# Kernel tuning notes

Hardware: AMD Instinct MI355X
Metric: run time of the kernel (lower is better)

Reference implementation:

```python
import jax, jax.numpy as jnp
import numpy as np


def setup_inputs() -> dict:
    key = jax.random.key(0)
    ks = jax.random.split(key, 12)
    N, F, H, E = 100000, 128, 128, 625000
    x = jax.random.normal(ks[0], (N, F), dtype=jnp.float32)
    edge_index = jax.random.randint(ks[1], (2, E), 0, N, dtype=jnp.int64)
    s1 = 1.0 / np.sqrt(2 * F)
    s2 = 1.0 / np.sqrt(H)
    W1 = jax.random.uniform(ks[2], (2 * F, H), jnp.float32, -s1, s1)
    b1 = jax.random.uniform(ks[3], (H,), jnp.float32, -s1, s1)
    W2 = jax.random.uniform(ks[4], (H, H), jnp.float32, -s2, s2)
    b2 = jax.random.uniform(ks[5], (H,), jnp.float32, -s2, s2)
    W3 = jax.random.uniform(ks[6], (H, H), jnp.float32, -s2, s2)
    b3 = jax.random.uniform(ks[7], (H,), jnp.float32, -s2, s2)
    W4 = jax.random.uniform(ks[8], (H, 1), jnp.float32, -s2, s2)
    b4 = jax.random.uniform(ks[9], (1,), jnp.float32, -s2, s2)
    return {"x": x, "edge_index": edge_index, "W1": W1, "b1": b1,
            "W2": W2, "b2": b2, "W3": W3, "b3": b3, "W4": W4, "b4": b4}


def reference(x, edge_index, W1, b1, W2, b2, W3, b3, W4, b4):
    # Gather endpoint features and concat -> [E, 2F]
    x_i = x[edge_index[0], :]
    x_j = x[edge_index[1], :]
    ef = jnp.concatenate([x_i, x_j], axis=-1)
    h = jax.nn.relu(ef @ W1 + b1)
    h = jax.nn.relu(h @ W2 + b2)
    h = jax.nn.relu(h @ W3 + b3)
    return jax.nn.sigmoid(h @ W4 + b4)  # [E, 1]
```

## Files before the change

### kernel.cpp

```cpp
#include <hip/hip_runtime.h>
#include <math.h>

typedef _Float16 half8 __attribute__((ext_vector_type(8)));
typedef _Float16 half4 __attribute__((ext_vector_type(4)));
typedef float f32x4 __attribute__((ext_vector_type(4)));

#define HDIM 128
#define WHALFS 65536
#define SCR_HALFS 2048
#define LDS_HALFS (WHALFS + 8 * SCR_HALFS)
#define LDS_BYTES (LDS_HALFS * 2)

__global__ __launch_bounds__(256) void prep_kernel(
    const float* __restrict__ x,  const float* __restrict__ W1,
    const float* __restrict__ W2, const float* __restrict__ W3,
    _Float16* __restrict__ xh,  _Float16* __restrict__ W1p,
    _Float16* __restrict__ W2p, _Float16* __restrict__ W3p, int NF)
{
    int bid = blockIdx.x;
    if (bid < 32) {
        int t = bid * 256 + threadIdx.x;
        const float* W; _Float16* Wp; int KS; int u;
        if (t < 4096)      { W = W1; Wp = W1p; KS = 8; u = t; }
        else if (t < 6144) { W = W2; Wp = W2p; KS = 4; u = t - 4096; }
        else               { W = W3; Wp = W3p; KS = 4; u = t - 6144; }
        int lane = u & 63;
        int fk   = u >> 6;
        int ks   = fk % KS;
        int ct   = fk / KS;
        int m    = ct * 16 + (lane & 15);
        int k0   = ks * 32 + (lane >> 4) * 8;
        half8 v;
        #pragma unroll
        for (int j = 0; j < 8; ++j) v[j] = (_Float16)W[(k0 + j) * HDIM + m];
        *(half8*)(Wp + (size_t)u * 8) = v;
    } else {
        const long stride = (long)(gridDim.x - 32) * 256;
        for (long u = (long)(bid - 32) * 256 + threadIdx.x; u * 8 < (long)NF; u += stride) {
            long i = u * 8;
            const float4* xf = (const float4*)(x + i);
            float4 f0 = xf[0], f1 = xf[1];
            half8 v;
            v[0] = (_Float16)f0.x; v[1] = (_Float16)f0.y;
            v[2] = (_Float16)f0.z; v[3] = (_Float16)f0.w;
            v[4] = (_Float16)f1.x; v[5] = (_Float16)f1.y;
            v[6] = (_Float16)f1.z; v[7] = (_Float16)f1.w;
            *(half8*)(xh + i) = v;
        }
    }
}

__device__ __forceinline__ void acc_bias_init(
    f32x4 (&acc)[2][8], const float* __restrict__ bias, int quad)
{
    #pragma unroll
    for (int ct = 0; ct < 8; ++ct) {
        float4 bv = *(const float4*)(bias + ct * 16 + quad * 4);
        f32x4 b = {bv.x, bv.y, bv.z, bv.w};
        acc[0][ct] = b;
        acc[1][ct] = b;
    }
}

__device__ __forceinline__ void epi_extract(
    f32x4 (&acc)[2][8], _Float16* __restrict__ scr, int l15, int quad, int sw,
    half8 (&bh)[2][4], const float* __restrict__ next_bias)
{
    #pragma unroll
    for (int nt = 0; nt < 2; ++nt) {
        #pragma unroll
        for (int ct = 0; ct < 8; ++ct) {
            half4 h;
            h[0] = (_Float16)fmaxf(acc[nt][ct][0], 0.f);
            h[1] = (_Float16)fmaxf(acc[nt][ct][1], 0.f);
            h[2] = (_Float16)fmaxf(acc[nt][ct][2], 0.f);
            h[3] = (_Float16)fmaxf(acc[nt][ct][3], 0.f);
            *(half4*)(scr + ((l15 * 128 + ct * 16 + quad * 4) ^ sw)) = h;
        }
        #pragma unroll
        for (int ks = 0; ks < 4; ++ks)
            bh[nt][ks] = *(const half8*)(scr + ((l15 * 128 + ks * 32 + quad * 8) ^ sw));
    }
    acc_bias_init(acc, next_bias, quad);
}

__device__ __forceinline__ void layer_mfma(
    f32x4 (&acc)[2][8], const _Float16* __restrict__ Wl,
    half8 (&bh)[2][4], int lane)
{
    __builtin_amdgcn_s_setprio(1);
    #pragma unroll
    for (int ks = 0; ks < 4; ++ks) {
        #pragma unroll
        for (int ch = 0; ch < 2; ++ch) {
            half8 aw[4];
            #pragma unroll
            for (int c = 0; c < 4; ++c)
                aw[c] = *(const half8*)(Wl + ((size_t)(((ch * 4 + c) * 4 + ks) * 64 + lane)) * 8);
            #pragma unroll
            for (int nt = 0; nt < 2; ++nt)
                #pragma unroll
                for (int c = 0; c < 4; ++c)
                    acc[nt][ch * 4 + c] = __builtin_amdgcn_mfma_f32_16x16x32_f16(
                        aw[c], bh[nt][ks], acc[nt][ch * 4 + c], 0, 0, 0);
        }
    }
    __builtin_amdgcn_s_setprio(0);
}

__device__ __forceinline__ void layer1_half(
    f32x4 (&acc)[2][8], const _Float16* __restrict__ W1l,
    half8 (&bef)[2][4], int ks0, int lane)
{
    __builtin_amdgcn_s_setprio(1);
    #pragma unroll
    for (int ks = 0; ks < 4; ++ks) {
        #pragma unroll
        for (int ch = 0; ch < 2; ++ch) {
            half8 aw[4];
            #pragma unroll
            for (int c = 0; c < 4; ++c)
                aw[c] = *(const half8*)(W1l + ((size_t)(((ch * 4 + c) * 8 + ks0 + ks) * 64 + lane)) * 8);
            #pragma unroll
            for (int nt = 0; nt < 2; ++nt)
                #pragma unroll
                for (int c = 0; c < 4; ++c)
                    acc[nt][ch * 4 + c] = __builtin_amdgcn_mfma_f32_16x16x32_f16(
                        aw[c], bef[nt][ks], acc[nt][ch * 4 + c], 0, 0, 0);
        }
    }
    __builtin_amdgcn_s_setprio(0);
}

__global__ __launch_bounds__(512, 2) void edge_mlp_kernel(
    const int* __restrict__ ei, const _Float16* __restrict__ xh,
    const _Float16* __restrict__ wpack,
    const float* __restrict__ b1, const float* __restrict__ b2,
    const float* __restrict__ b3, const float* __restrict__ W4,
    const float* __restrict__ b4, float* __restrict__ out, int E)
{
    extern __shared__ _Float16 lds[];

    {
        float4* dst = (float4*)lds;
        const float4* src = (const float4*)wpack;
        #pragma unroll
        for (int i = 0; i < 16; ++i)
            dst[i * 512 + threadIdx.x] = src[i * 512 + threadIdx.x];
    }
    __syncthreads();

    const int tid  = threadIdx.x;
    const int wave = tid >> 6;
    const int lane = tid & 63;
    const int l15  = lane & 15;
    const int quad = lane >> 4;
    const int sw   = (l15 & 7) << 3;

    const _Float16* W1l = lds;
    const _Float16* W2l = lds + 32768;
    const _Float16* W3l = lds + 49152;
    _Float16* scr = lds + WHALFS + wave * SCR_HALFS;

    const int ntiles = (E + 255) >> 8;
    const float b4v = b4[0];

    int gi[2], gj[2];
    {
        const int base0 = blockIdx.x * 256 + wave * 32;
        #pragma unroll
        for (int nt = 0; nt < 2; ++nt) {
            const int row = min(base0 + nt * 16 + l15, E - 1);
            gi[nt] = ei[row];
            gj[nt] = ei[E + row];
        }
    }

    for (int t = blockIdx.x; t < ntiles; t += gridDim.x) {
        const int base = t * 256 + wave * 32;

        half8 befi[2][4], befj[2][4];
        #pragma unroll
        for (int nt = 0; nt < 2; ++nt) {
            const _Float16* pi = xh + (size_t)gi[nt] * HDIM;
            #pragma unroll
            for (int ks = 0; ks < 4; ++ks)
                befi[nt][ks] = *(const half8*)(pi + ks * 32 + quad * 8);
        }
        #pragma unroll
        for (int nt = 0; nt < 2; ++nt) {
            const _Float16* pj = xh + (size_t)gj[nt] * HDIM;
            #pragma unroll
            for (int ks = 0; ks < 4; ++ks)
                befj[nt][ks] = *(const half8*)(pj + ks * 32 + quad * 8);
        }
        int gin[2], gjn[2];
        {
            const int basen = min(t + (int)gridDim.x, ntiles - 1) * 256 + wave * 32;
            #pragma unroll
            for (int nt = 0; nt < 2; ++nt) {
                const int row = min(basen + nt * 16 + l15, E - 1);
                gin[nt] = ei[row];
                gjn[nt] = ei[E + row];
            }
        }

        f32x4 acc[2][8];
        acc_bias_init(acc, b1, quad);

        layer1_half(acc, W1l, befi, 0, lane);
        layer1_half(acc, W1l, befj, 4, lane);

        half8 bh[2][4];
        epi_extract(acc, scr, l15, quad, sw, bh, b2);
        layer_mfma(acc, W2l, bh, lane);
        epi_extract(acc, scr, l15, quad, sw, bh, b3);
        layer_mfma(acc, W3l, bh, lane);

        #pragma unroll
        for (int nt = 0; nt < 2; ++nt) {
            float s = 0.f;
            #pragma unroll
            for (int ct = 0; ct < 8; ++ct) {
                float4 w4v = *(const float4*)(W4 + ct * 16 + quad * 4);
                s += fmaxf(acc[nt][ct][0], 0.f) * w4v.x;
                s += fmaxf(acc[nt][ct][1], 0.f) * w4v.y;
                s += fmaxf(acc[nt][ct][2], 0.f) * w4v.z;
                s += fmaxf(acc[nt][ct][3], 0.f) * w4v.w;
            }
            s += __shfl_xor(s, 16, 64);
            s += __shfl_xor(s, 32, 64);
            const int row = base + nt * 16 + l15;
            if (quad == 0 && row < E)
                out[row] = 1.f / (1.f + __expf(-(s + b4v)));
        }

        gi[0] = gin[0]; gi[1] = gin[1];
        gj[0] = gjn[0]; gj[1] = gjn[1];
    }
}

extern "C" void kernel_launch(void* const* d_in, const int* in_sizes, int n_in,
                              void* d_out, int out_size, void* d_ws, size_t ws_size,
                              hipStream_t stream)
{
    const float* x  = (const float*)d_in[0];
    const int*   ei = (const int*)d_in[1];
    const float* W1 = (const float*)d_in[2];
    const float* b1 = (const float*)d_in[3];
    const float* W2 = (const float*)d_in[4];
    const float* b2 = (const float*)d_in[5];
    const float* W3 = (const float*)d_in[6];
    const float* b3 = (const float*)d_in[7];
    const float* W4 = (const float*)d_in[8];
    const float* b4 = (const float*)d_in[9];
    float* out = (float*)d_out;

    const int NF = 100000 * 128;
    const int E  = out_size;

    _Float16* xh  = (_Float16*)d_ws;
    _Float16* W1p = xh + NF;
    _Float16* W2p = W1p + 32768;
    _Float16* W3p = W2p + 16384;

    prep_kernel<<<32 + 2048, 256, 0, stream>>>(x, W1, W2, W3, xh, W1p, W2p, W3p, NF);

    hipFuncSetAttribute((const void*)edge_mlp_kernel,
                        hipFuncAttributeMaxDynamicSharedMemorySize, LDS_BYTES);
    edge_mlp_kernel<<<256, 512, LDS_BYTES, stream>>>(ei, xh, W1p,
                                                     b1, b2, b3, W4, b4, out, E);
}
```

Baseline: 207.5 us.

## Switch to 32x32x16 MFMA with register-shuffle epilogue and async LDS gather

Changes the MLP matmuls from 16x16x32 to 32x32x16 MFMA tiles, one 32-edge tile per wave, and repacks the weights to match. The inter-layer ReLU/fp16 conversion now uses a cross-half-wave shuffle instead of an LDS scratch round-trip. Part of the x_j gather goes through global_load_lds to overlap with layer-1 MFMAs, and the next index prefetch moves later. The intent is fewer LDS operations and better MFMA efficiency and latency hiding, at the cost of a new register layout and an explicit vmcnt wait.

```diff
diff --git a/kernel.cpp b/kernel.cpp
--- a/kernel.cpp
+++ b/kernel.cpp
@@ -2,8 +2,9 @@
 #include <math.h>
 
 typedef _Float16 half8 __attribute__((ext_vector_type(8)));
-typedef _Float16 half4 __attribute__((ext_vector_type(4)));
+typedef _Float16 half2v __attribute__((ext_vector_type(2)));
 typedef float f32x4 __attribute__((ext_vector_type(4)));
+typedef float f32x16 __attribute__((ext_vector_type(16)));
 
 #define HDIM 128
 #define WHALFS 65536
@@ -11,6 +12,13 @@
 #define LDS_HALFS (WHALFS + 8 * SCR_HALFS)
 #define LDS_BYTES (LDS_HALFS * 2)
 
+__device__ __forceinline__ void gld_lds16(const _Float16* g, _Float16* l)
+{
+    __builtin_amdgcn_global_load_lds(
+        (const __attribute__((address_space(1))) void*)g,
+        (__attribute__((address_space(3))) void*)l, 16, 0, 0);
+}
+
 __global__ __launch_bounds__(256) void prep_kernel(
     const float* __restrict__ x,  const float* __restrict__ W1,
     const float* __restrict__ W2, const float* __restrict__ W3,
@@ -21,15 +29,15 @@
     if (bid < 32) {
         int t = bid * 256 + threadIdx.x;
         const float* W; _Float16* Wp; int KS; int u;
-        if (t < 4096)      { W = W1; Wp = W1p; KS = 8; u = t; }
-        else if (t < 6144) { W = W2; Wp = W2p; KS = 4; u = t - 4096; }
-        else               { W = W3; Wp = W3p; KS = 4; u = t - 6144; }
+        if (t < 4096)      { W = W1; Wp = W1p; KS = 16; u = t; }
+        else if (t < 6144) { W = W2; Wp = W2p; KS = 8;  u = t - 4096; }
+        else               { W = W3; Wp = W3p; KS = 8;  u = t - 6144; }
         int lane = u & 63;
         int fk   = u >> 6;
         int ks   = fk % KS;
-        int ct   = fk / KS;
-        int m    = ct * 16 + (lane & 15);
-        int k0   = ks * 32 + (lane >> 4) * 8;
+        int mt   = fk / KS;
+        int m    = mt * 32 + (lane & 31);
+        int k0   = ks * 16 + (lane >> 5) * 8;
         half8 v;
         #pragma unroll
         for (int j = 0; j < 8; ++j) v[j] = (_Float16)W[(k0 + j) * HDIM + m];
@@ -51,83 +59,84 @@
 }
 
 __device__ __forceinline__ void acc_bias_init(
-    f32x4 (&acc)[2][8], const float* __restrict__ bias, int quad)
+    f32x16 (&acc)[4], const float* __restrict__ bias, int H)
 {
     #pragma unroll
-    for (int ct = 0; ct < 8; ++ct) {
-        float4 bv = *(const float4*)(bias + ct * 16 + quad * 4);
-        f32x4 b = {bv.x, bv.y, bv.z, bv.w};
-        acc[0][ct] = b;
-        acc[1][ct] = b;
-    }
-}
-
-__device__ __forceinline__ void epi_extract(
-    f32x4 (&acc)[2][8], _Float16* __restrict__ scr, int l15, int quad, int sw,
-    half8 (&bh)[2][4], const float* __restrict__ next_bias)
+    for (int mt = 0; mt < 4; ++mt)
+        #pragma unroll
+        for (int g = 0; g < 4; ++g) {
+            float4 bv = *(const float4*)(bias + mt * 32 + g * 8 + H * 4);
+            acc[mt][4 * g + 0] = bv.x;
+            acc[mt][4 * g + 1] = bv.y;
+            acc[mt][4 * g + 2] = bv.z;
+            acc[mt][4 * g + 3] = bv.w;
+        }
+}
+
+__device__ __forceinline__ void epi_exchange(
+    f32x16 (&acc)[4], half8 (&bh)[8], int H)
 {
     #pragma unroll
-    for (int nt = 0; nt < 2; ++nt) {
-        #pragma unroll
-        for (int ct = 0; ct < 8; ++ct) {
-            half4 h;
-            h[0] = (_Float16)fmaxf(acc[nt][ct][0], 0.f);
-            h[1] = (_Float16)fmaxf(acc[nt][ct][1], 0.f);
-            h[2] = (_Float16)fmaxf(acc[nt][ct][2], 0.f);
-            h[3] = (_Float16)fmaxf(acc[nt][ct][3], 0.f);
-            *(half4*)(scr + ((l15 * 128 + ct * 16 + quad * 4) ^ sw)) = h;
-        }
-        #pragma unroll
-        for (int ks = 0; ks < 4; ++ks)
-            bh[nt][ks] = *(const half8*)(scr + ((l15 * 128 + ks * 32 + quad * 8) ^ sw));
-    }
-    acc_bias_init(acc, next_bias, quad);
+    for (int mt = 0; mt < 4; ++mt) {
+        unsigned w[8], pw[8];
+        #pragma unroll
+        for (int g = 0; g < 8; ++g) {
+            union { half2v v; unsigned u; } cv;
+            cv.v[0] = (_Float16)fmaxf(acc[mt][2 * g],     0.f);
+            cv.v[1] = (_Float16)fmaxf(acc[mt][2 * g + 1], 0.f);
+            w[g] = cv.u;
+        }
+        #pragma unroll
+        for (int g = 0; g < 8; ++g)
+            pw[g] = (unsigned)__shfl_xor((int)w[g], 32, 64);
+        union { unsigned u[4]; half8 h; } f0, f1;
+        f0.u[0] = H ? pw[2] : w[0];
+        f0.u[1] = H ? pw[3] : w[1];
+        f0.u[2] = H ? w[2]  : pw[0];
+        f0.u[3] = H ? w[3]  : pw[1];
+        f1.u[0] = H ? pw[6] : w[4];
+        f1.u[1] = H ? pw[7] : w[5];
+        f1.u[2] = H ? w[6]  : pw[4];
+        f1.u[3] = H ? w[7]  : pw[5];
+        bh[2 * mt]     = f0.h;
+        bh[2 * mt + 1] = f1.h;
+    }
 }
 
 __device__ __forceinline__ void layer_mfma(
-    f32x4 (&acc)[2][8], const _Float16* __restrict__ Wl,
-    half8 (&bh)[2][4], int lane)
+    f32x16 (&acc)[4], const _Float16* __restrict__ Wl,
+    half8 (&bh)[8], int lane)
+{
+    __builtin_amdgcn_s_setprio(1);
+    #pragma unroll
+    for (int ks = 0; ks < 8; ++ks) {
+        half8 aw[4];
+        #pragma unroll
+        for (int mt = 0; mt < 4; ++mt)
+            aw[mt] = *(const half8*)(Wl + ((size_t)((mt * 8 + ks) * 64 + lane)) * 8);
+        #pragma unroll
+        for (int mt = 0; mt < 4; ++mt)
+            acc[mt] = __builtin_amdgcn_mfma_f32_32x32x16_f16(
+                aw[mt], bh[ks], acc[mt], 0, 0, 0);
+    }
+    __builtin_amdgcn_s_setprio(0);
+}
+
+__device__ __forceinline__ void l1_chunk(
+    f32x16 (&acc)[4], const _Float16* __restrict__ W1l,
+    half8 (&bef)[4], int ks0, int lane)
 {
     __builtin_amdgcn_s_setprio(1);
     #pragma unroll
     for (int ks = 0; ks < 4; ++ks) {
-        #pragma unroll
-        for (int ch = 0; ch < 2; ++ch) {
-            half8 aw[4];
-            #pragma unroll
-            for (int c = 0; c < 4; ++c)
-                aw[c] = *(const half8*)(Wl + ((size_t)(((ch * 4 + c) * 4 + ks) * 64 + lane)) * 8);
-            #pragma unroll
-            for (int nt = 0; nt < 2; ++nt)
-                #pragma unroll
-                for (int c = 0; c < 4; ++c)
-                    acc[nt][ch * 4 + c] = __builtin_amdgcn_mfma_f32_16x16x32_f16(
-                        aw[c], bh[nt][ks], acc[nt][ch * 4 + c], 0, 0, 0);
-        }
-    }
-    __builtin_amdgcn_s_setprio(0);
-}
-
-__device__ __forceinline__ void layer1_half(
-    f32x4 (&acc)[2][8], const _Float16* __restrict__ W1l,
-    half8 (&bef)[2][4], int ks0, int lane)
-{
-    __builtin_amdgcn_s_setprio(1);
-    #pragma unroll
-    for (int ks = 0; ks < 4; ++ks) {
-        #pragma unroll
-        for (int ch = 0; ch < 2; ++ch) {
-            half8 aw[4];
-            #pragma unroll
-            for (int c = 0; c < 4; ++c)
-                aw[c] = *(const half8*)(W1l + ((size_t)(((ch * 4 + c) * 8 + ks0 + ks) * 64 + lane)) * 8);
-            #pragma unroll
-            for (int nt = 0; nt < 2; ++nt)
-                #pragma unroll
-                for (int c = 0; c < 4; ++c)
-                    acc[nt][ch * 4 + c] = __builtin_amdgcn_mfma_f32_16x16x32_f16(
-                        aw[c], bef[nt][ks], acc[nt][ch * 4 + c], 0, 0, 0);
-        }
+        half8 aw[4];
+        #pragma unroll
+        for (int mt = 0; mt < 4; ++mt)
+            aw[mt] = *(const half8*)(W1l + ((size_t)((mt * 16 + ks0 + ks) * 64 + lane)) * 8);
+        #pragma unroll
+        for (int mt = 0; mt < 4; ++mt)
+            acc[mt] = __builtin_amdgcn_mfma_f32_32x32x16_f16(
+                aw[mt], bef[ks], acc[mt], 0, 0, 0);
     }
     __builtin_amdgcn_s_setprio(0);
 }
@@ -153,9 +162,8 @@
     const int tid  = threadIdx.x;
     const int wave = tid >> 6;
     const int lane = tid & 63;
-    const int l15  = lane & 15;
-    const int quad = lane >> 4;
-    const int sw   = (l15 & 7) << 3;
+    const int e32  = lane & 31;
+    const int H    = lane >> 5;
 
     const _Float16* W1l = lds;
     const _Float16* W2l = lds + 32768;
@@ -165,78 +173,105 @@
     const int ntiles = (E + 255) >> 8;
     const float b4v = b4[0];
 
-    int gi[2], gj[2];
+    int gi, gj;
     {
-        const int base0 = blockIdx.x * 256 + wave * 32;
-        #pragma unroll
-        for (int nt = 0; nt < 2; ++nt) {
-            const int row = min(base0 + nt * 16 + l15, E - 1);
-            gi[nt] = ei[row];
-            gj[nt] = ei[E + row];
-        }
+        const int row = min(blockIdx.x * 256 + wave * 32 + e32, E - 1);
+        gi = ei[row];
+        gj = ei[E + row];
     }
 
     for (int t = blockIdx.x; t < ntiles; t += gridDim.x) {
         const int base = t * 256 + wave * 32;
 
-        half8 befi[2][4], befj[2][4];
-        #pragma unroll
-        for (int nt = 0; nt < 2; ++nt) {
-            const _Float16* pi = xh + (size_t)gi[nt] * HDIM;
-            #pragma unroll
-            for (int ks = 0; ks < 4; ++ks)
-                befi[nt][ks] = *(const half8*)(pi + ks * 32 + quad * 8);
-        }
-        #pragma unroll
-        for (int nt = 0; nt < 2; ++nt) {
-            const _Float16* pj = xh + (size_t)gj[nt] * HDIM;
-            #pragma unroll
-            for (int ks = 0; ks < 4; ++ks)
-                befj[nt][ks] = *(const half8*)(pj + ks * 32 + quad * 8);
-        }
-        int gin[2], gjn[2];
-        {
-            const int basen = min(t + (int)gridDim.x, ntiles - 1) * 256 + wave * 32;
-            #pragma unroll
-            for (int nt = 0; nt < 2; ++nt) {
-                const int row = min(basen + nt * 16 + l15, E - 1);
-                gin[nt] = ei[row];
-                gjn[nt] = ei[E + row];
-            }
-        }
-
-        f32x4 acc[2][8];
-        acc_bias_init(acc, b1, quad);
-
-        layer1_half(acc, W1l, befi, 0, lane);
-        layer1_half(acc, W1l, befj, 4, lane);
-
-        half8 bh[2][4];
-        epi_extract(acc, scr, l15, quad, sw, bh, b2);
+        {
+            const _Float16* pj = xh + (size_t)gj * HDIM + 64 + H * 8;
+            #pragma unroll
+            for (int c = 0; c < 4; ++c)
+                gld_lds16(pj + c * 16, scr + c * 512);
+        }
+
+        half8 bef[4];
+        {
+            const _Float16* pi = xh + (size_t)gi * HDIM + H * 8;
+            #pragma unroll
+            for (int c = 0; c < 4; ++c)
+                bef[c] = *(const half8*)(pi + c * 16);
+        }
+
+        f32x16 acc[4];
+        acc_bias_init(acc, b1, H);
+
+        half8 befB[4];
+        {
+            const _Float16* pi = xh + (size_t)gi * HDIM + 64 + H * 8;
+            #pragma unroll
+            for (int c = 0; c < 4; ++c)
+                befB[c] = *(const half8*)(pi + c * 16);
+        }
+        l1_chunk(acc, W1l, bef, 0, lane);
+
+        {
+            const _Float16* pj = xh + (size_t)gj * HDIM + H * 8;
+            #pragma unroll
+            for (int c = 0; c < 4; ++c)
+                bef[c] = *(const half8*)(pj + c * 16);
+        }
+        l1_chunk(acc, W1l, befB, 4, lane);
+
+        l1_chunk(acc, W1l, bef, 8, lane);
+
+        asm volatile("s_waitcnt vmcnt(0)" ::: "memory");
+        __builtin_amdgcn_s_setprio(1);
+        #pragma unroll
+        for (int c = 0; c < 4; ++c) {
+            half8 bj = *(const half8*)(scr + c * 512 + lane * 8);
+            half8 aw[4];
+            #pragma unroll
+            for (int mt = 0; mt < 4; ++mt)
+                aw[mt] = *(const half8*)(W1l + ((size_t)((mt * 16 + 12 + c) * 64 + lane)) * 8);
+            #pragma unroll
+            for (int mt = 0; mt < 4; ++mt)
+                acc[mt] = __builtin_amdgcn_mfma_f32_32x32x16_f16(
+                    aw[mt], bj, acc[mt], 0, 0, 0);
+        }
+        __builtin_amdgcn_s_setprio(0);
+
+        half8 bh[8];
+        epi_exchange(acc, bh, H);
+        acc_bias_init(acc, b2, H);
+
+        int gin, gjn;
+        {
+            const int rown = min(min(t + (int)gridDim.x, ntiles - 1) * 256
+                                 + wave * 32 + e32, E - 1);
+            gin = ei[rown];
+            gjn = ei[E + rown];
+        }
+
         layer_mfma(acc, W2l, bh, lane);
-        epi_extract(acc, scr, l15, quad, sw, bh, b3);
+        epi_exchange(acc, bh, H);
+        acc_bias_init(acc, b3, H);
         layer_mfma(acc, W3l, bh, lane);
 
-        #pragma unroll
-        for (int nt = 0; nt < 2; ++nt) {
+        {
             float s = 0.f;
             #pragma unroll
-            for (int ct = 0; ct < 8; ++ct) {
-                float4 w4v = *(const float4*)(W4 + ct * 16 + quad * 4);
-                s += fmaxf(acc[nt][ct][0], 0.f) * w4v.x;
-                s += fmaxf(acc[nt][ct][1], 0.f) * w4v.y;
-                s += fmaxf(acc[nt][ct][2], 0.f) * w4v.z;
-                s += fmaxf(acc[nt][ct][3], 0.f) * w4v.w;
-            }
-            s += __shfl_xor(s, 16, 64);
+            for (int mt = 0; mt < 4; ++mt)
+                #pragma unroll
+                for (int g = 0; g < 4; ++g) {
+                    float4 w4v = *(const float4*)(W4 + mt * 32 + g * 8 + H * 4);
+                    s += fmaxf(acc[mt][4 * g + 0], 0.f) * w4v.x;
+                    s += fmaxf(acc[mt][4 * g + 1], 0.f) * w4v.y;
+                    s += fmaxf(acc[mt][4 * g + 2], 0.f) * w4v.z;
+                    s += fmaxf(acc[mt][4 * g + 3], 0.f) * w4v.w;
+                }
             s += __shfl_xor(s, 32, 64);
-            const int row = base + nt * 16 + l15;
-            if (quad == 0 && row < E)
+            const int row = base + e32;
+            if (lane < 32 && row < E)
                 out[row] = 1.f / (1.f + __expf(-(s + b4v)));
         }
 
-        gi[0] = gin[0]; gi[1] = gin[1];
-        gj[0] = gjn[0]; gj[1] = gjn[1];
+        gi = gin; gj = gjn;
     }
 }
 
```

Result: no change. 203.6 us (-1.9%).
